# Kernel tuning notes

Hardware: AMD Instinct MI355X
Metric: run time of the kernel (lower is better)

## Reference

```python
import jax, jax.numpy as jnp
import numpy as np

N_NODES = 50000
N_EDGES = 800000
NFEAT = 128
NHID = 64  # gc1: NFEAT -> 2*NHID, gc2: 2*NHID -> NHID


def setup_inputs() -> dict:
    key = jax.random.key(0)
    k1, k2, k3, k4, k5 = jax.random.split(key, 5)
    feat = jax.random.normal(k1, (N_NODES, NFEAT), dtype=jnp.float32)
    src = jax.random.randint(k2, (N_EDGES,), 0, N_NODES, dtype=jnp.int32)
    dst = jax.random.randint(k3, (N_EDGES,), 0, N_NODES, dtype=jnp.int32)
    # GraphConv weights: (in_feats, out_feats), xavier-like scale
    W1 = jax.random.normal(k4, (NFEAT, 2 * NHID), dtype=jnp.float32) / np.sqrt(NFEAT)
    b1 = jnp.zeros((2 * NHID,), dtype=jnp.float32)
    W2 = jax.random.normal(k5, (2 * NHID, NHID), dtype=jnp.float32) / np.sqrt(2 * NHID)
    b2 = jnp.zeros((NHID,), dtype=jnp.float32)
    return {"feat": feat, "src": src, "dst": dst, "W1": W1, "b1": b1, "W2": W2, "b2": b2}


def _graph_conv(feat, src, dst, W, b):
    """DGL GraphConv, norm='both', allow_zero_in_degree=True.
    h = D_in^{-1/2} A (D_out^{-1/2} x) W + b, with degrees clamped to >= 1.
    Applies W before aggregation when in_feats > out_feats (saves bandwidth)."""
    N = feat.shape[0]
    ones = jnp.ones(src.shape[0], dtype=feat.dtype)
    deg_out = jnp.clip(jax.ops.segment_sum(ones, src, num_segments=N), 1.0)
    deg_in = jnp.clip(jax.ops.segment_sum(ones, dst, num_segments=N), 1.0)
    h = feat * (deg_out ** -0.5)[:, None]
    mult_first = W.shape[0] > W.shape[1]
    if mult_first:
        h = h @ W
    agg = jax.ops.segment_sum(h[src], dst, num_segments=N)  # [N, d]
    if not mult_first:
        agg = agg @ W
    return agg * (deg_in ** -0.5)[:, None] + b


def reference(feat, src, dst, W1, b1, W2, b2):
    x = jax.nn.relu(_graph_conv(feat, src, dst, W1, b1))
    # dropout is inactive in eval mode (F.dropout training=False)
    x = _graph_conv(x, src, dst, W2, b2)
    return jax.nn.log_softmax(x, axis=1)
```

## Files before the change

### kernel.cpp

```cpp
#include <hip/hip_runtime.h>
#include <math.h>


constexpr int NF   = 128;
constexpr int NH   = 64;
constexpr int CAP  = 48;
constexpr int EPB  = 4096;
constexpr int BCAP = 8192;
constexpr int NBKMAX = 256;

typedef unsigned int uint;
typedef unsigned short ushort_t;
typedef __attribute__((ext_vector_type(8))) short short8;
typedef __attribute__((ext_vector_type(4))) float f32x4;

__device__ __forceinline__ float bflo(uint u) { return __uint_as_float(u << 16); }
__device__ __forceinline__ float bfhi(uint u) { return __uint_as_float(u & 0xffff0000u); }
__device__ __forceinline__ uint packbf(float a, float b) {
    uint ua = __float_as_uint(a), ub = __float_as_uint(b);
    uint ra = (ua + 0x7fffu + ((ua >> 16) & 1u)) >> 16;
    uint rb = (ub + 0x7fffu + ((ub >> 16) & 1u)) >> 16;
    return ra | (rb << 16);
}
__device__ __forceinline__ ushort_t bf16u(float f) {
    uint u = __float_as_uint(f);
    return (ushort_t)((u + 0x7fffu + ((u >> 16) & 1u)) >> 16);
}
__device__ __forceinline__ short8 as_short8(uint4 u) {
    union { uint4 u; short8 s; } x; x.u = u; return x.s;
}

__global__ __launch_bounds__(1024) void partition_kernel(
        const int* __restrict__ src, const int* __restrict__ dst,
        uint* __restrict__ pairs_g, ushort_t* __restrict__ srcb_g,
        int* __restrict__ dcur, int* __restrict__ scur,
        int E, int nbk) {
    __shared__ uint     pl[EPB];
    __shared__ ushort_t sl[EPB];
    __shared__ int dh[NBKMAX], sh[NBKMAX];
    __shared__ int doff[NBKMAX], soff[NBKMAX];
    __shared__ int dbase[NBKMAX], sbase[NBKMAX];
    __shared__ int dpos[NBKMAX], spos[NBKMAX];
    int tid = threadIdx.x;
    int e0 = blockIdx.x * EPB;
    int ecnt = min(EPB, E - e0);

    for (int b = tid; b < nbk; b += 1024) { dh[b] = 0; sh[b] = 0; }
    __syncthreads();
    for (int i = tid; i < ecnt; i += 1024) {
        atomicAdd(&dh[dst[e0 + i] >> 8], 1);
        atomicAdd(&sh[src[e0 + i] >> 8], 1);
    }
    __syncthreads();
    if (tid == 0)  { int run = 0; for (int b = 0; b < nbk; ++b) { doff[b] = run; run += dh[b]; } }
    if (tid == 64) { int run = 0; for (int b = 0; b < nbk; ++b) { soff[b] = run; run += sh[b]; } }
    for (int b = tid; b < nbk; b += 1024) {
        dbase[b] = atomicAdd(&dcur[b], dh[b]);
        sbase[b] = atomicAdd(&scur[b], sh[b]);
    }
    __syncthreads();
    for (int b = tid; b < nbk; b += 1024) { dpos[b] = doff[b]; spos[b] = soff[b]; }
    __syncthreads();
    for (int i = tid; i < ecnt; i += 1024) {
        int s = src[e0 + i], d = dst[e0 + i];
        int p = atomicAdd(&dpos[d >> 8], 1);
        pl[p] = ((uint)s << 16) | (uint)d;
        int q = atomicAdd(&spos[s >> 8], 1);
        sl[q] = (ushort_t)s;
    }
    __syncthreads();
    for (int i = tid; i < ecnt; i += 1024) {
        uint e = pl[i];
        int b = (int)((e & 0xffffu) >> 8);
        int gp = dbase[b] + (i - doff[b]);
        if (gp < BCAP) pairs_g[(size_t)b * BCAP + gp] = e;
        ushort_t sv = sl[i];
        int b2 = (int)(sv >> 8);
        int gq = sbase[b2] + (i - soff[b2]);
        if (gq < BCAP) srcb_g[(size_t)b2 * BCAP + gq] = sv;
    }
}

__global__ __launch_bounds__(1024) void bin_kernel(
        const uint* __restrict__ pairs_g, const ushort_t* __restrict__ srcb_g,
        const int* __restrict__ dcur, const int* __restrict__ scur,
        const float* __restrict__ feat, uint* __restrict__ featb,
        ushort_t* __restrict__ slots, int* __restrict__ lens,
        float* __restrict__ s_in, float* __restrict__ s_out, int N) {
    __shared__ ushort_t slots_l[256 * CAP];
    __shared__ int cin[256], cout[256];
    __shared__ float souts[256];
    int tid = threadIdx.x;
    int b = blockIdx.x;
    int lo = b << 8;
    for (int r = tid; r < 256; r += 1024) { cin[r] = 0; cout[r] = 0; }
    __syncthreads();
    int dn = min(dcur[b], BCAP);
    for (int i = tid; i < dn; i += 1024) {
        uint e = pairs_g[(size_t)b * BCAP + i];
        int r = (int)(e & 255u);
        int p = atomicAdd(&cin[r], 1);
        if (p < CAP) slots_l[r * CAP + p] = (ushort_t)(e >> 16);
    }
    int sn = min(scur[b], BCAP);
    for (int i = tid; i < sn; i += 1024)
        atomicAdd(&cout[(int)srcb_g[(size_t)b * BCAP + i] - lo], 1);
    __syncthreads();
    int nrow = min(256, N - lo);
    {
        const uint4* sl4 = (const uint4*)slots_l;
        uint4* gs4 = (uint4*)(slots + (size_t)lo * CAP);
        int lim4 = nrow * (CAP / 8);
        for (int k = tid; k < 256 * CAP / 8; k += 1024)
            if (k < lim4) gs4[k] = sl4[k];
    }
    for (int r = tid; r < nrow; r += 1024) {
        int node = lo + r;
        int ci = cin[r];
        lens[node]  = min(ci, CAP);
        s_in[node]  = rsqrtf((float)max(ci, 1));
        float so    = rsqrtf((float)max(cout[r], 1));
        s_out[node] = so;
        souts[r]    = so;
    }
    __syncthreads();
    for (int k = tid; k < nrow * 16; k += 1024) {
        int r = k >> 4, ch = k & 15;
        float sc = souts[r];
        const float4* f4 = (const float4*)(feat + (size_t)(lo + r) * NF + ch * 8);
        float4 a = f4[0], c = f4[1];
        uint4 o;
        o.x = packbf(a.x * sc, a.y * sc);
        o.y = packbf(a.z * sc, a.w * sc);
        o.z = packbf(c.x * sc, c.y * sc);
        o.w = packbf(c.z * sc, c.w * sc);
        *(uint4*)(featb + (size_t)(lo + r) * 64 + ch * 4) = o;
    }
}

__global__ __launch_bounds__(256) void cast_w_kernel(
        const float* __restrict__ W1, const float* __restrict__ W2,
        uint* __restrict__ W1p, uint* __restrict__ W2p) {
    int i = blockIdx.x * 256 + threadIdx.x;
    if (i < 8192) {
        int jp = i & 3, g = (i >> 2) & 3, n = (i >> 4) & 127, kk = i >> 11;
        int k = kk * 32 + g * 8 + jp * 2;
        W1p[i] = packbf(W1[k * 128 + n], W1[(k + 1) * 128 + n]);
    } else if (i < 12288) {
        int j = i - 8192;
        int jp = j & 3, g = (j >> 2) & 3, n = (j >> 4) & 63, kk = j >> 10;
        int k = kk * 32 + g * 8 + jp * 2;
        W2p[j] = packbf(W2[k * 64 + n], W2[(k + 1) * 64 + n]);
    }
}

__global__ __launch_bounds__(256) void agg1_kernel(const uint* __restrict__ featb,
        const int* __restrict__ lens, const ushort_t* __restrict__ slots,
        uint* __restrict__ agg1b, int N) {
    int wave = threadIdx.x >> 6;
    int lane = threadIdx.x & 63;
    int q   = lane >> 4;
    int sub = lane & 15;
    int node = blockIdx.x * 4 + wave;
    if (node >= N) return;
    int beg = node * CAP;
    int len = lens[node];
    float acc[8] = {0.f, 0.f, 0.f, 0.f, 0.f, 0.f, 0.f, 0.f};
    if (len > 0) {
        int li = min(lane, len - 1);
        int sidx = (int)slots[beg + li];
        int quads = (len + 3) >> 2;
        #pragma unroll 4
        for (int k = 0; k < quads; ++k) {
            int e = 4 * k + q;
            int s = __shfl(sidx, e, 64);
            if (e < len) {
                uint4 v = *(const uint4*)(featb + (size_t)s * 64 + sub * 4);
                acc[0] += bflo(v.x); acc[1] += bfhi(v.x);
                acc[2] += bflo(v.y); acc[3] += bfhi(v.y);
                acc[4] += bflo(v.z); acc[5] += bfhi(v.z);
                acc[6] += bflo(v.w); acc[7] += bfhi(v.w);
            }
        }
    }
    #pragma unroll
    for (int j = 0; j < 8; ++j) {
        acc[j] += __shfl_xor(acc[j], 32, 64);
        acc[j] += __shfl_xor(acc[j], 16, 64);
    }
    if (q == 0) {
        uint4 o;
        o.x = packbf(acc[0], acc[1]);
        o.y = packbf(acc[2], acc[3]);
        o.z = packbf(acc[4], acc[5]);
        o.w = packbf(acc[6], acc[7]);
        *(uint4*)(agg1b + (size_t)node * 64 + sub * 4) = o;
    }
}

__global__ __launch_bounds__(256) void fused_gemm_kernel(
        const uint* __restrict__ agg1b, const uint* __restrict__ W1p,
        const float* __restrict__ b1, const uint* __restrict__ W2p,
        const float* __restrict__ s_in, const float* __restrict__ s_out,
        uint* __restrict__ h2b, int N) {
    __shared__ ushort_t x1t[64][136];
    __shared__ float sin_l[64], sout_l[64];
    int t = threadIdx.x;
    int base = blockIdx.x * 64;
    int w    = t >> 6;
    int lane = t & 63;
    int c = lane & 15;
    int g = lane >> 4;

    if (t < 64)       sin_l[t]        = (base + t < N) ? s_in[base + t] : 0.f;
    else if (t < 128) sout_l[t - 64]  = (base + t - 64 < N) ? s_out[base + t - 64] : 0.f;
    __syncthreads();

    f32x4 zero = {0.f, 0.f, 0.f, 0.f};
    f32x4 c1[4][2];
    #pragma unroll
    for (int mt = 0; mt < 4; ++mt) { c1[mt][0] = zero; c1[mt][1] = zero; }
    #pragma unroll
    for (int kk = 0; kk < 4; ++kk) {
        short8 bf[2];
        #pragma unroll
        for (int ntl = 0; ntl < 2; ++ntl) {
            int n = (2 * w + ntl) * 16 + c;
            bf[ntl] = as_short8(*(const uint4*)(W1p + (size_t)kk * 2048 + n * 16 + g * 4));
        }
        #pragma unroll
        for (int mt = 0; mt < 4; ++mt) {
            int row = base + mt * 16 + c;
            short8 af = as_short8(*(const uint4*)(agg1b + (size_t)row * 64 + kk * 16 + g * 4));
            c1[mt][0] = __builtin_amdgcn_mfma_f32_16x16x32_bf16(af, bf[0], c1[mt][0], 0, 0, 0);
            c1[mt][1] = __builtin_amdgcn_mfma_f32_16x16x32_bf16(af, bf[1], c1[mt][1], 0, 0, 0);
        }
    }
    float bias0 = b1[(2 * w) * 16 + c];
    float bias1 = b1[(2 * w + 1) * 16 + c];
    #pragma unroll
    for (int mt = 0; mt < 4; ++mt) {
        #pragma unroll
        for (int r = 0; r < 4; ++r) {
            int rl = mt * 16 + g * 4 + r;
            float si = sin_l[rl], so = sout_l[rl];
            x1t[rl][(2 * w) * 16 + c]     = bf16u(fmaxf(fmaf(si, c1[mt][0][r], bias0), 0.f) * so);
            x1t[rl][(2 * w + 1) * 16 + c] = bf16u(fmaxf(fmaf(si, c1[mt][1][r], bias1), 0.f) * so);
        }
    }
    __syncthreads();

    f32x4 c2[4];
    #pragma unroll
    for (int mt = 0; mt < 4; ++mt) c2[mt] = zero;
    #pragma unroll
    for (int kk = 0; kk < 4; ++kk) {
        int n = w * 16 + c;
        short8 bf2 = as_short8(*(const uint4*)(W2p + (size_t)kk * 1024 + n * 16 + g * 4));
        #pragma unroll
        for (int mt = 0; mt < 4; ++mt) {
            short8 af = *(const short8*)&x1t[mt * 16 + c][kk * 32 + g * 8];
            c2[mt] = __builtin_amdgcn_mfma_f32_16x16x32_bf16(af, bf2, c2[mt], 0, 0, 0);
        }
    }
    __syncthreads();

    ushort_t* h2t = &x1t[0][0];
    #pragma unroll
    for (int mt = 0; mt < 4; ++mt) {
        #pragma unroll
        for (int r = 0; r < 4; ++r) {
            int rl = mt * 16 + g * 4 + r;
            h2t[rl * 72 + w * 16 + c] = bf16u(c2[mt][r]);
        }
    }
    __syncthreads();
    int row = t >> 2, ch = t & 3;
    if (base + row < N) {
        uint4 v0 = *(const uint4*)(h2t + row * 72 + ch * 16);
        uint4 v1 = *(const uint4*)(h2t + row * 72 + ch * 16 + 8);
        *(uint4*)(h2b + (size_t)(base + row) * 32 + ch * 8)     = v0;
        *(uint4*)(h2b + (size_t)(base + row) * 32 + ch * 8 + 4) = v1;
    }
}

__global__ __launch_bounds__(256) void agg2_softmax_kernel(const uint* __restrict__ h2b,
        const int* __restrict__ lens, const ushort_t* __restrict__ slots,
        const float* __restrict__ s_in, const float* __restrict__ b2,
        float* __restrict__ out, int N) {
    int wave = threadIdx.x >> 6;
    int lane = threadIdx.x & 63;
    int oct = lane >> 3;
    int sub = lane & 7;
    int node = blockIdx.x * 4 + wave;
    if (node >= N) return;
    int beg = node * CAP;
    int len = lens[node];
    float acc[8] = {0.f, 0.f, 0.f, 0.f, 0.f, 0.f, 0.f, 0.f};
    if (len > 0) {
        int li = min(lane, len - 1);
        int sidx = (int)slots[beg + li];
        int octs = (len + 7) >> 3;
        #pragma unroll 4
        for (int k = 0; k < octs; ++k) {
            int e = 8 * k + oct;
            int s = __shfl(sidx, e, 64);
            if (e < len) {
                uint4 v = *(const uint4*)(h2b + (size_t)s * 32 + sub * 4);
                acc[0] += bflo(v.x); acc[1] += bfhi(v.x);
                acc[2] += bflo(v.y); acc[3] += bfhi(v.y);
                acc[4] += bflo(v.z); acc[5] += bfhi(v.z);
                acc[6] += bflo(v.w); acc[7] += bfhi(v.w);
            }
        }
    }
    #pragma unroll
    for (int j = 0; j < 8; ++j) {
        acc[j] += __shfl_xor(acc[j], 32, 64);
        acc[j] += __shfl_xor(acc[j], 16, 64);
        acc[j] += __shfl_xor(acc[j], 8, 64);
    }
    float si = s_in[node];
    float4 bb0 = *(const float4*)(b2 + sub * 8);
    float4 bb1 = *(const float4*)(b2 + sub * 8 + 4);
    float v[8];
    v[0] = fmaf(acc[0], si, bb0.x); v[1] = fmaf(acc[1], si, bb0.y);
    v[2] = fmaf(acc[2], si, bb0.z); v[3] = fmaf(acc[3], si, bb0.w);
    v[4] = fmaf(acc[4], si, bb1.x); v[5] = fmaf(acc[5], si, bb1.y);
    v[6] = fmaf(acc[6], si, bb1.z); v[7] = fmaf(acc[7], si, bb1.w);

    float m = v[0];
    #pragma unroll
    for (int j = 1; j < 8; ++j) m = fmaxf(m, v[j]);
    m = fmaxf(m, __shfl_xor(m, 4, 64));
    m = fmaxf(m, __shfl_xor(m, 2, 64));
    m = fmaxf(m, __shfl_xor(m, 1, 64));
    float s8 = 0.f;
    #pragma unroll
    for (int j = 0; j < 8; ++j) s8 += expf(v[j] - m);
    s8 += __shfl_xor(s8, 4, 64);
    s8 += __shfl_xor(s8, 2, 64);
    s8 += __shfl_xor(s8, 1, 64);
    float ls = m + logf(s8);
    if (oct == 0) {
        float4 o0 = make_float4(v[0] - ls, v[1] - ls, v[2] - ls, v[3] - ls);
        float4 o1 = make_float4(v[4] - ls, v[5] - ls, v[6] - ls, v[7] - ls);
        *(float4*)(out + (size_t)node * NH + sub * 8)     = o0;
        *(float4*)(out + (size_t)node * NH + sub * 8 + 4) = o1;
    }
}

extern "C" void kernel_launch(void* const* d_in, const int* in_sizes, int n_in,
                              void* d_out, int out_size, void* d_ws, size_t ws_size,
                              hipStream_t stream) {
    const float* feat = (const float*)d_in[0];
    const int*   src  = (const int*)d_in[1];
    const int*   dst  = (const int*)d_in[2];
    const float* W1   = (const float*)d_in[3];
    const float* b1   = (const float*)d_in[4];
    const float* W2   = (const float*)d_in[5];
    const float* b2   = (const float*)d_in[6];
    float* out = (float*)d_out;

    int N = in_sizes[0] / NF;
    int E = in_sizes[1];
    int nbk = (N + 255) >> 8;
    int nchunk = (E + EPB - 1) / EPB;
    int Npad = (N + 63) & ~63;

    char* p = (char*)d_ws;
    auto alloc = [&](size_t bytes) -> char* {
        char* q = p;
        p += (bytes + 255) & ~(size_t)255;
        return q;
    };
    int*      dcur  = (int*)alloc((size_t)nbk * 4);
    int*      scur  = (int*)alloc((size_t)nbk * 4);
    uint*     pairs = (uint*)alloc((size_t)nbk * BCAP * 4);
    ushort_t* srcb  = (ushort_t*)alloc((size_t)nbk * BCAP * 2);
    ushort_t* slots = (ushort_t*)alloc((size_t)N * CAP * 2);
    int*      lens  = (int*)alloc((size_t)N * 4);
    float*    s_out = (float*)alloc((size_t)N * 4);
    float*    s_in  = (float*)alloc((size_t)N * 4);
    uint*     featb = (uint*)alloc((size_t)N * 64 * 4);
    uint*     agg1b = (uint*)alloc((size_t)Npad * 64 * 4);
    uint*     W1p   = (uint*)alloc(8192 * 4);
    uint*     W2p   = (uint*)alloc(4096 * 4);
    uint*     h2b   = (uint*)alloc((size_t)N * 32 * 4);

    size_t cur_span = (size_t)((char*)scur - (char*)dcur) + (size_t)nbk * 4;
    hipMemsetAsync(dcur, 0, cur_span, stream);

    partition_kernel<<<nchunk, 1024, 0, stream>>>(src, dst, pairs, srcb, dcur, scur, E, nbk);
    cast_w_kernel<<<48, 256, 0, stream>>>(W1, W2, W1p, W2p);
    bin_kernel<<<nbk, 1024, 0, stream>>>(pairs, srcb, dcur, scur, feat, featb,
                                         slots, lens, s_in, s_out, N);
    agg1_kernel<<<(N + 3) / 4, 256, 0, stream>>>(featb, lens, slots, agg1b, N);
    fused_gemm_kernel<<<(N + 63) / 64, 256, 0, stream>>>(agg1b, W1p, b1, W2p, s_in, s_out, h2b, N);
    agg2_softmax_kernel<<<(N + 3) / 4, 256, 0, stream>>>(h2b, lens, slots, s_in, b2, out, N);
}
```

Before: 176.9 us.

## Fuse layer-1 aggregation into GEMM kernel and fold weight cast into partition

Merges the layer-1 neighbor gather-sum into the fused GEMM kernel. Each 1024-thread block aggregates 64 nodes into shared memory and then runs both MFMA GEMMs on that tile, so the agg1b round trip through global memory and one launch go away. The weight bf16 packing now runs as 12 extra blocks appended to the partition kernel, which removes another launch. In exchange the aggregation phase sits in larger blocks with a barrier before the GEMM, which may reduce occupancy and overlap of gather latency.

Result: no change. 178.8 us (+1.1%).

```diff
diff --git a/kernel.cpp b/kernel.cpp
--- a/kernel.cpp
+++ b/kernel.cpp
@@ -34,7 +34,23 @@
         const int* __restrict__ src, const int* __restrict__ dst,
         uint* __restrict__ pairs_g, ushort_t* __restrict__ srcb_g,
         int* __restrict__ dcur, int* __restrict__ scur,
-        int E, int nbk) {
+        const float* __restrict__ W1, const float* __restrict__ W2,
+        uint* __restrict__ W1p, uint* __restrict__ W2p,
+        int E, int nbk, int nchunk) {
+    if (blockIdx.x >= nchunk) {
+        int i = (blockIdx.x - nchunk) * 1024 + threadIdx.x;
+        if (i < 8192) {
+            int jp = i & 3, g = (i >> 2) & 3, n = (i >> 4) & 127, kk = i >> 11;
+            int k = kk * 32 + g * 8 + jp * 2;
+            W1p[i] = packbf(W1[k * 128 + n], W1[(k + 1) * 128 + n]);
+        } else if (i < 12288) {
+            int j = i - 8192;
+            int jp = j & 3, g = (j >> 2) & 3, n = (j >> 4) & 63, kk = j >> 10;
+            int k = kk * 32 + g * 8 + jp * 2;
+            W2p[j] = packbf(W2[k * 64 + n], W2[(k + 1) * 64 + n]);
+        }
+        return;
+    }
     __shared__ uint     pl[EPB];
     __shared__ ushort_t sl[EPB];
     __shared__ int dh[NBKMAX], sh[NBKMAX];
@@ -138,149 +154,114 @@
     }
 }
 
-__global__ __launch_bounds__(256) void cast_w_kernel(
-        const float* __restrict__ W1, const float* __restrict__ W2,
-        uint* __restrict__ W1p, uint* __restrict__ W2p) {
-    int i = blockIdx.x * 256 + threadIdx.x;
-    if (i < 8192) {
-        int jp = i & 3, g = (i >> 2) & 3, n = (i >> 4) & 127, kk = i >> 11;
-        int k = kk * 32 + g * 8 + jp * 2;
-        W1p[i] = packbf(W1[k * 128 + n], W1[(k + 1) * 128 + n]);
-    } else if (i < 12288) {
-        int j = i - 8192;
-        int jp = j & 3, g = (j >> 2) & 3, n = (j >> 4) & 63, kk = j >> 10;
-        int k = kk * 32 + g * 8 + jp * 2;
-        W2p[j] = packbf(W2[k * 64 + n], W2[(k + 1) * 64 + n]);
-    }
-}
-
-__global__ __launch_bounds__(256) void agg1_kernel(const uint* __restrict__ featb,
-        const int* __restrict__ lens, const ushort_t* __restrict__ slots,
-        uint* __restrict__ agg1b, int N) {
-    int wave = threadIdx.x >> 6;
-    int lane = threadIdx.x & 63;
-    int q   = lane >> 4;
-    int sub = lane & 15;
-    int node = blockIdx.x * 4 + wave;
-    if (node >= N) return;
-    int beg = node * CAP;
-    int len = lens[node];
-    float acc[8] = {0.f, 0.f, 0.f, 0.f, 0.f, 0.f, 0.f, 0.f};
-    if (len > 0) {
-        int li = min(lane, len - 1);
-        int sidx = (int)slots[beg + li];
-        int quads = (len + 3) >> 2;
-        #pragma unroll 4
-        for (int k = 0; k < quads; ++k) {
-            int e = 4 * k + q;
-            int s = __shfl(sidx, e, 64);
-            if (e < len) {
-                uint4 v = *(const uint4*)(featb + (size_t)s * 64 + sub * 4);
-                acc[0] += bflo(v.x); acc[1] += bfhi(v.x);
-                acc[2] += bflo(v.y); acc[3] += bfhi(v.y);
-                acc[4] += bflo(v.z); acc[5] += bfhi(v.z);
-                acc[6] += bflo(v.w); acc[7] += bfhi(v.w);
-            }
-        }
-    }
-    #pragma unroll
-    for (int j = 0; j < 8; ++j) {
-        acc[j] += __shfl_xor(acc[j], 32, 64);
-        acc[j] += __shfl_xor(acc[j], 16, 64);
-    }
-    if (q == 0) {
-        uint4 o;
-        o.x = packbf(acc[0], acc[1]);
-        o.y = packbf(acc[2], acc[3]);
-        o.z = packbf(acc[4], acc[5]);
-        o.w = packbf(acc[6], acc[7]);
-        *(uint4*)(agg1b + (size_t)node * 64 + sub * 4) = o;
-    }
-}
-
-__global__ __launch_bounds__(256) void fused_gemm_kernel(
-        const uint* __restrict__ agg1b, const uint* __restrict__ W1p,
+__global__ __launch_bounds__(1024) void agg_gemm_kernel(
+        const uint* __restrict__ featb, const int* __restrict__ lens,
+        const ushort_t* __restrict__ slots, const uint* __restrict__ W1p,
         const float* __restrict__ b1, const uint* __restrict__ W2p,
         const float* __restrict__ s_in, const float* __restrict__ s_out,
         uint* __restrict__ h2b, int N) {
+    __shared__ uint aggt[64 * 68];
     __shared__ ushort_t x1t[64][136];
     __shared__ float sin_l[64], sout_l[64];
     int t = threadIdx.x;
     int base = blockIdx.x * 64;
-    int w    = t >> 6;
+    int wv   = t >> 6;
     int lane = t & 63;
-    int c = lane & 15;
-    int g = lane >> 4;
-
-    if (t < 64)       sin_l[t]        = (base + t < N) ? s_in[base + t] : 0.f;
-    else if (t < 128) sout_l[t - 64]  = (base + t - 64 < N) ? s_out[base + t - 64] : 0.f;
-    __syncthreads();
-
+    int q = lane >> 4, sub = lane & 15;
+
+    if (t < 64)       sin_l[t]       = (base + t < N) ? s_in[base + t] : 0.f;
+    else if (t < 128) sout_l[t - 64] = (base + t - 64 < N) ? s_out[base + t - 64] : 0.f;
+
+    for (int i = 0; i < 4; ++i) {
+        int nl = wv * 4 + i;
+        int node = base + nl;
+        float acc[8] = {0.f, 0.f, 0.f, 0.f, 0.f, 0.f, 0.f, 0.f};
+        if (node < N) {
+            int len = lens[node];
+            if (len > 0) {
+                int beg = node * CAP;
+                int li = min(lane, len - 1);
+                int sidx = (int)slots[beg + li];
+                int quads = (len + 3) >> 2;
+                #pragma unroll 4
+                for (int k = 0; k < quads; ++k) {
+                    int e = 4 * k + q;
+                    int s = __shfl(sidx, e, 64);
+                    if (e < len) {
+                        uint4 v = *(const uint4*)(featb + (size_t)s * 64 + sub * 4);
+                        acc[0] += bflo(v.x); acc[1] += bfhi(v.x);
+                        acc[2] += bflo(v.y); acc[3] += bfhi(v.y);
+                        acc[4] += bflo(v.z); acc[5] += bfhi(v.z);
+                        acc[6] += bflo(v.w); acc[7] += bfhi(v.w);
+                    }
+                }
+            }
+        }
+        #pragma unroll
+        for (int j = 0; j < 8; ++j) {
+            acc[j] += __shfl_xor(acc[j], 32, 64);
+            acc[j] += __shfl_xor(acc[j], 16, 64);
+        }
+        if (q == 0) {
+            uint4 o;
+            o.x = packbf(acc[0], acc[1]);
+            o.y = packbf(acc[2], acc[3]);
+            o.z = packbf(acc[4], acc[5]);
+            o.w = packbf(acc[6], acc[7]);
+            *(uint4*)&aggt[nl * 68 + sub * 4] = o;
+        }
+    }
+    __syncthreads();
+
+    int c = lane & 15, g = lane >> 4;
+    int mt = wv & 3, ng = wv >> 2;
     f32x4 zero = {0.f, 0.f, 0.f, 0.f};
-    f32x4 c1[4][2];
-    #pragma unroll
-    for (int mt = 0; mt < 4; ++mt) { c1[mt][0] = zero; c1[mt][1] = zero; }
+    f32x4 c1[2] = {zero, zero};
     #pragma unroll
     for (int kk = 0; kk < 4; ++kk) {
         short8 bf[2];
         #pragma unroll
         for (int ntl = 0; ntl < 2; ++ntl) {
-            int n = (2 * w + ntl) * 16 + c;
+            int n = (2 * ng + ntl) * 16 + c;
             bf[ntl] = as_short8(*(const uint4*)(W1p + (size_t)kk * 2048 + n * 16 + g * 4));
         }
-        #pragma unroll
-        for (int mt = 0; mt < 4; ++mt) {
-            int row = base + mt * 16 + c;
-            short8 af = as_short8(*(const uint4*)(agg1b + (size_t)row * 64 + kk * 16 + g * 4));
-            c1[mt][0] = __builtin_amdgcn_mfma_f32_16x16x32_bf16(af, bf[0], c1[mt][0], 0, 0, 0);
-            c1[mt][1] = __builtin_amdgcn_mfma_f32_16x16x32_bf16(af, bf[1], c1[mt][1], 0, 0, 0);
-        }
-    }
-    float bias0 = b1[(2 * w) * 16 + c];
-    float bias1 = b1[(2 * w + 1) * 16 + c];
-    #pragma unroll
-    for (int mt = 0; mt < 4; ++mt) {
+        short8 af = as_short8(*(const uint4*)&aggt[(mt * 16 + c) * 68 + kk * 16 + g * 4]);
+        c1[0] = __builtin_amdgcn_mfma_f32_16x16x32_bf16(af, bf[0], c1[0], 0, 0, 0);
+        c1[1] = __builtin_amdgcn_mfma_f32_16x16x32_bf16(af, bf[1], c1[1], 0, 0, 0);
+    }
+    #pragma unroll
+    for (int ntl = 0; ntl < 2; ++ntl) {
+        float bias = b1[(2 * ng + ntl) * 16 + c];
         #pragma unroll
         for (int r = 0; r < 4; ++r) {
             int rl = mt * 16 + g * 4 + r;
-            float si = sin_l[rl], so = sout_l[rl];
-            x1t[rl][(2 * w) * 16 + c]     = bf16u(fmaxf(fmaf(si, c1[mt][0][r], bias0), 0.f) * so);
-            x1t[rl][(2 * w + 1) * 16 + c] = bf16u(fmaxf(fmaf(si, c1[mt][1][r], bias1), 0.f) * so);
-        }
-    }
-    __syncthreads();
-
-    f32x4 c2[4];
-    #pragma unroll
-    for (int mt = 0; mt < 4; ++mt) c2[mt] = zero;
+            x1t[rl][(2 * ng + ntl) * 16 + c] =
+                bf16u(fmaxf(fmaf(sin_l[rl], c1[ntl][r], bias), 0.f) * sout_l[rl]);
+        }
+    }
+    __syncthreads();
+
+    int mt2 = wv & 3, nt2 = wv >> 2;
+    f32x4 c2 = zero;
     #pragma unroll
     for (int kk = 0; kk < 4; ++kk) {
-        int n = w * 16 + c;
-        short8 bf2 = as_short8(*(const uint4*)(W2p + (size_t)kk * 1024 + n * 16 + g * 4));
-        #pragma unroll
-        for (int mt = 0; mt < 4; ++mt) {
-            short8 af = *(const short8*)&x1t[mt * 16 + c][kk * 32 + g * 8];
-            c2[mt] = __builtin_amdgcn_mfma_f32_16x16x32_bf16(af, bf2, c2[mt], 0, 0, 0);
-        }
-    }
-    __syncthreads();
-
-    ushort_t* h2t = &x1t[0][0];
-    #pragma unroll
-    for (int mt = 0; mt < 4; ++mt) {
-        #pragma unroll
-        for (int r = 0; r < 4; ++r) {
-            int rl = mt * 16 + g * 4 + r;
-            h2t[rl * 72 + w * 16 + c] = bf16u(c2[mt][r]);
-        }
-    }
-    __syncthreads();
-    int row = t >> 2, ch = t & 3;
-    if (base + row < N) {
-        uint4 v0 = *(const uint4*)(h2t + row * 72 + ch * 16);
-        uint4 v1 = *(const uint4*)(h2t + row * 72 + ch * 16 + 8);
-        *(uint4*)(h2b + (size_t)(base + row) * 32 + ch * 8)     = v0;
-        *(uint4*)(h2b + (size_t)(base + row) * 32 + ch * 8 + 4) = v1;
+        short8 bf2 = as_short8(*(const uint4*)(W2p + (size_t)kk * 1024 + (nt2 * 16 + c) * 16 + g * 4));
+        short8 af = *(const short8*)&x1t[mt2 * 16 + c][kk * 32 + g * 8];
+        c2 = __builtin_amdgcn_mfma_f32_16x16x32_bf16(af, bf2, c2, 0, 0, 0);
+    }
+    ushort_t* h2t = (ushort_t*)aggt;
+    #pragma unroll
+    for (int r = 0; r < 4; ++r) {
+        int rl = mt2 * 16 + g * 4 + r;
+        h2t[rl * 72 + nt2 * 16 + c] = bf16u(c2[r]);
+    }
+    __syncthreads();
+    if (t < 512) {
+        int row = t >> 3, ch = t & 7;
+        if (base + row < N) {
+            uint4 v = *(const uint4*)(h2t + row * 72 + ch * 8);
+            *(uint4*)(h2b + (size_t)(base + row) * 32 + ch * 4) = v;
+        }
     }
 }
 
@@ -366,7 +347,6 @@
     int E = in_sizes[1];
     int nbk = (N + 255) >> 8;
     int nchunk = (E + EPB - 1) / EPB;
-    int Npad = (N + 63) & ~63;
 
     char* p = (char*)d_ws;
     auto alloc = [&](size_t bytes) -> char* {
@@ -383,7 +363,6 @@
     float*    s_out = (float*)alloc((size_t)N * 4);
     float*    s_in  = (float*)alloc((size_t)N * 4);
     uint*     featb = (uint*)alloc((size_t)N * 64 * 4);
-    uint*     agg1b = (uint*)alloc((size_t)Npad * 64 * 4);
     uint*     W1p   = (uint*)alloc(8192 * 4);
     uint*     W2p   = (uint*)alloc(4096 * 4);
     uint*     h2b   = (uint*)alloc((size_t)N * 32 * 4);
@@ -391,11 +370,11 @@
     size_t cur_span = (size_t)((char*)scur - (char*)dcur) + (size_t)nbk * 4;
     hipMemsetAsync(dcur, 0, cur_span, stream);
 
-    partition_kernel<<<nchunk, 1024, 0, stream>>>(src, dst, pairs, srcb, dcur, scur, E, nbk);
-    cast_w_kernel<<<48, 256, 0, stream>>>(W1, W2, W1p, W2p);
+    partition_kernel<<<nchunk + 12, 1024, 0, stream>>>(
+        src, dst, pairs, srcb, dcur, scur, W1, W2, W1p, W2p, E, nbk, nchunk);
     bin_kernel<<<nbk, 1024, 0, stream>>>(pairs, srcb, dcur, scur, feat, featb,
                                          slots, lens, s_in, s_out, N);
-    agg1_kernel<<<(N + 3) / 4, 256, 0, stream>>>(featb, lens, slots, agg1b, N);
-    fused_gemm_kernel<<<(N + 63) / 64, 256, 0, stream>>>(agg1b, W1p, b1, W2p, s_in, s_out, h2b, N);
+    agg_gemm_kernel<<<(N + 63) / 64, 1024, 0, stream>>>(
+        featb, lens, slots, W1p, b1, W2p, s_in, s_out, h2b, N);
     agg2_softmax_kernel<<<(N + 3) / 4, 256, 0, stream>>>(h2b, lens, slots, s_in, b2, out, N);
 }
```
